# Optimization experiments

Hardware: AMD Instinct MI355X
Metric: run time of the kernel (lower is better)

Reference implementation:

```python
import jax, jax.numpy as jnp
import numpy as np

D = 1024
H = 16
FF = 4 * D


def layer_norm(x, g, b, eps=1e-5):
    mu = jnp.mean(x, axis=-1, keepdims=True)
    var = jnp.var(x, axis=-1, keepdims=True)
    return (x - mu) * jax.lax.rsqrt(var + eps) * g + b


def setup_inputs() -> dict:
    key = jax.random.key(0)
    ks = jax.random.split(key, 8)
    s = lambda fan_in: 1.0 / np.sqrt(fan_in)
    return {
        "x": jax.random.normal(ks[0], (2, 2048, D), dtype=jnp.float32),
        "ln1_g": jnp.ones((D,), jnp.float32),
        "ln1_b": jnp.zeros((D,), jnp.float32),
        "w_qkv": jax.random.uniform(ks[1], (D, 3 * D), jnp.float32, -s(D), s(D)),
        "b_qkv": jnp.zeros((3 * D,), jnp.float32),
        "w_out": jax.random.uniform(ks[2], (D, D), jnp.float32, -s(D), s(D)),
        "b_out": jnp.zeros((D,), jnp.float32),
        "ln2_g": jnp.ones((D,), jnp.float32),
        "ln2_b": jnp.zeros((D,), jnp.float32),
        "w_fc1": jax.random.uniform(ks[3], (D, FF), jnp.float32, -s(D), s(D)),
        "b_fc1": jnp.zeros((FF,), jnp.float32),
        "w_fc2": jax.random.uniform(ks[4], (FF, D), jnp.float32, -s(FF), s(FF)),
        "b_fc2": jnp.zeros((D,), jnp.float32),
    }


def reference(x, ln1_g, ln1_b, w_qkv, b_qkv, w_out, b_out,
              ln2_g, ln2_b, w_fc1, b_fc1, w_fc2, b_fc2):
    b, n, c = x.shape
    hd = c // H
    scale = hd ** -0.5

    # --- pre-norm MHA ---
    h = layer_norm(x, ln1_g, ln1_b)
    qkv = h @ w_qkv + b_qkv                      # [b,n,3c]
    qkv = qkv.reshape(b, n, 3, H, hd)
    q = jnp.transpose(qkv[:, :, 0], (0, 2, 1, 3))  # [b,H,n,hd]
    k = jnp.transpose(qkv[:, :, 1], (0, 2, 1, 3))
    v = jnp.transpose(qkv[:, :, 2], (0, 2, 1, 3))
    attn = jnp.einsum('bhqd,bhkd->bhqk', q, k) * scale
    attn = jax.nn.softmax(attn, axis=-1)
    o = jnp.einsum('bhqk,bhkd->bhqd', attn, v)   # [b,H,n,hd]
    o = jnp.transpose(o, (0, 2, 1, 3)).reshape(b, n, c)
    x = x + (o @ w_out + b_out)

    # --- pre-norm FFN ---
    h = layer_norm(x, ln2_g, ln2_b)
    h = jax.nn.gelu(h @ w_fc1 + b_fc1, approximate=False)
    x = x + (h @ w_fc2 + b_fc2)
    return x
```

## Files before the change

### kernel.cpp

```cpp
#include <hip/hip_runtime.h>
#include <stdint.h>
#include <math.h>

#define D_MODEL 1024
#define NHEAD   16
#define HDIM    64
#define FFDIM   4096
#define SEQ     2048
#define BATCH   2
#define NTOK    (BATCH*SEQ)
#define QKVN    (3*D_MODEL)

typedef __bf16 bf16;
typedef __attribute__((ext_vector_type(8))) __bf16 bf16x8;
typedef __attribute__((ext_vector_type(4))) __bf16 bf16x4;
typedef __attribute__((ext_vector_type(4))) float f32x4;

__device__ __forceinline__ void gld_lds16(const void* g, void* l) {
    __builtin_amdgcn_global_load_lds((__attribute__((address_space(1))) void*)g,
                                     (__attribute__((address_space(3))) void*)l,
                                     16, 0, 0);
}

__device__ __forceinline__ float fast_exp2(float x) {
#if __has_builtin(__builtin_amdgcn_exp2f)
    return __builtin_amdgcn_exp2f(x);
#else
    return __expf(x * 0.69314718056f);
#endif
}

__device__ __forceinline__ float fast_rcp(float x) {
#if __has_builtin(__builtin_amdgcn_rcpf)
    return __builtin_amdgcn_rcpf(x);
#else
    return 1.0f / x;
#endif
}

__device__ __forceinline__ float gelu_fast(float x) {
    float xx = x * x;
    float y  = x * fmaf(0.035677408137f, xx, 0.7978845608f);
    float z  = fminf(-2.8853900817779268f * y, 126.0f);
    float e  = fast_exp2(z);
    return x * fast_rcp(1.0f + e);
}

#define PHASE_BAR() do {                                       \
    asm volatile("s_waitcnt vmcnt(0)" ::: "memory");           \
    __builtin_amdgcn_s_barrier();                              \
    asm volatile("" ::: "memory");                             \
} while (0)

#define GEMM_BAR() do {                                        \
    asm volatile("s_waitcnt lgkmcnt(0)" ::: "memory");         \
    __builtin_amdgcn_s_barrier();                              \
    asm volatile("" ::: "memory");                             \
} while (0)

__global__ __launch_bounds__(256)
void k_transpose_all(const float* __restrict__ w_qkv, const float* __restrict__ w_out,
                     const float* __restrict__ w_fc1, const float* __restrict__ w_fc2,
                     bf16* __restrict__ t_qkv, bf16* __restrict__ t_out,
                     bf16* __restrict__ t_fc1, bf16* __restrict__ t_fc2) {
    __shared__ float tile[32][33];
    int bid = blockIdx.x;
    const float* W; bf16* Wt; int K, N, ti;
    if (bid < 3072)       { W = w_qkv; Wt = t_qkv; K = 1024; N = 3072; ti = bid; }
    else if (bid < 4096)  { W = w_out; Wt = t_out; K = 1024; N = 1024; ti = bid - 3072; }
    else if (bid < 8192)  { W = w_fc1; Wt = t_fc1; K = 1024; N = 4096; ti = bid - 4096; }
    else                  { W = w_fc2; Wt = t_fc2; K = 4096; N = 1024; ti = bid - 8192; }
    int tn = N >> 5;
    int n0 = (ti % tn) * 32, k0 = (ti / tn) * 32;
    int tx = threadIdx.x, ty = threadIdx.y;
#pragma unroll
    for (int i = 0; i < 4; i++)
        tile[ty + i * 8][tx] = W[(size_t)(k0 + ty + i * 8) * N + n0 + tx];
    __syncthreads();
#pragma unroll
    for (int i = 0; i < 4; i++)
        Wt[(size_t)(n0 + ty + i * 8) * K + k0 + tx] = (bf16)tile[tx][ty + i * 8];
}

__global__ __launch_bounds__(256)
void k_vtrans(const bf16* __restrict__ qkv, bf16* __restrict__ vT) {
    __shared__ bf16 t[32][33];
    int tok0 = blockIdx.x * 32, f0 = blockIdx.y * 32;
    int tx = threadIdx.x, ty = threadIdx.y;
#pragma unroll
    for (int i = 0; i < 4; i++)
        t[ty + i * 8][tx] = qkv[(size_t)(tok0 + ty + i * 8) * QKVN + 2 * D_MODEL + f0 + tx];
    __syncthreads();
    int s = tx;
    int pp = (s < 16) ? ((s >> 2) * 8 + (s & 3))
                      : (((s - 16) >> 2) * 8 + ((s - 16) & 3) + 4);
#pragma unroll
    for (int i = 0; i < 4; i++)
        vT[(size_t)(f0 + ty + i * 8) * NTOK + tok0 + pp] = t[tx][ty + i * 8];
}

__global__ __launch_bounds__(256)
void k_layernorm(const float* __restrict__ x, const float* __restrict__ g,
                 const float* __restrict__ b, bf16* __restrict__ out) {
    int row = blockIdx.x;
    int tid = threadIdx.x;
    float4 v = ((const float4*)(x + (size_t)row * D_MODEL))[tid];
    float s  = v.x + v.y + v.z + v.w;
    float ss = v.x * v.x + v.y * v.y + v.z * v.z + v.w * v.w;
#pragma unroll
    for (int off = 32; off > 0; off >>= 1) {
        s  += __shfl_down(s, off, 64);
        ss += __shfl_down(ss, off, 64);
    }
    __shared__ float red[2][4];
    __shared__ float mv[2];
    int wave = tid >> 6, lane = tid & 63;
    if (lane == 0) { red[0][wave] = s; red[1][wave] = ss; }
    __syncthreads();
    if (tid == 0) {
        float S  = red[0][0] + red[0][1] + red[0][2] + red[0][3];
        float SS = red[1][0] + red[1][1] + red[1][2] + red[1][3];
        float mu = S * (1.0f / D_MODEL);
        float var = SS * (1.0f / D_MODEL) - mu * mu;
        mv[0] = mu;
        mv[1] = rsqrtf(var + 1e-5f);
    }
    __syncthreads();
    float mu = mv[0], rs = mv[1];
    float4 gv = ((const float4*)g)[tid];
    float4 bv = ((const float4*)b)[tid];
    bf16x4 ov = { (bf16)((v.x - mu) * rs * gv.x + bv.x),
                  (bf16)((v.y - mu) * rs * gv.y + bv.y),
                  (bf16)((v.z - mu) * rs * gv.z + bv.z),
                  (bf16)((v.w - mu) * rs * gv.w + bv.w) };
    *(bf16x4*)(out + (size_t)row * D_MODEL + tid * 4) = ov;
}

template <int DO_GELU, int DO_RES, int OUT_BF16, int BN, int PIPE2, int SPLITK, int STAGE>
__global__ __launch_bounds__(256)
void k_gemm(const bf16* __restrict__ A, const bf16* __restrict__ Bt,
            const float* __restrict__ bias, const float* __restrict__ res,
            float* __restrict__ outf, bf16* __restrict__ outb,
            int M, int N, int K) {
    constexpr int WN = BN / 32;
    __shared__ bf16 As[2][128 * 32];
    __shared__ bf16 Bs[2][BN * 32];
    int tid  = threadIdx.x;
    int wave = tid >> 6, lane = tid & 63;
    int quad = lane >> 4, l16 = lane & 15;

    int nwg = gridDim.x * gridDim.y;
    int bid = blockIdx.y * gridDim.x + blockIdx.x;
    int sid = (bid & 7) * (nwg >> 3) + (bid >> 3);
    int bx = sid % gridDim.x, by = sid / gridDim.x;
    int m0 = by * 128, n0 = bx * BN;
    int wm = (wave >> 1) * 64, wn = (wave & 1) * (BN / 2);

    int Keff = (SPLITK == 2) ? (K >> 1) : K;
    int koff = (SPLITK == 2) ? blockIdx.z * Keff : 0;

    f32x4 acc[4][WN];
#pragma unroll
    for (int i = 0; i < 4; i++)
#pragma unroll
        for (int j = 0; j < WN; j++) acc[i][j] = (f32x4){0.f, 0.f, 0.f, 0.f};

    int lrow = lane >> 2;
    int lcol = (lane & 3) * 8;
    const bf16* gA0 = A + (size_t)(m0 + wave * 32 + lrow) * K + koff + lcol;
    const bf16* gA1 = gA0 + (size_t)16 * K;
    const bf16* gB0;
    const bf16* gB1 = nullptr;
    if constexpr (BN == 128) {
        gB0 = Bt + (size_t)(n0 + wave * 32 + lrow) * K + koff + lcol;
        gB1 = gB0 + (size_t)16 * K;
    } else {
        gB0 = Bt + (size_t)(n0 + wave * 16 + lrow) * K + koff + lcol;
    }

    int wA0 = wave * 1024 + lane * 8;
    int wA1 = wA0 + 512;
    int wB0 = (BN == 128) ? (wave * 1024 + lane * 8) : (wave * 512 + lane * 8);
    int wB1 = wB0 + 512;

    auto issue = [&](bf16x8* r, int k0) {
        r[0] = *(const bf16x8*)(gA0 + k0);
        r[1] = *(const bf16x8*)(gA1 + k0);
        r[2] = *(const bf16x8*)(gB0 + k0);
        if constexpr (BN == 128) r[3] = *(const bf16x8*)(gB1 + k0);
    };
    auto commit = [&](int buf, const bf16x8* r) {
        *(bf16x8*)(&As[buf][wA0]) = r[0];
        *(bf16x8*)(&As[buf][wA1]) = r[1];
        *(bf16x8*)(&Bs[buf][wB0]) = r[2];
        if constexpr (BN == 128) *(bf16x8*)(&Bs[buf][wB1]) = r[3];
    };
    auto compute = [&](const bf16* cA, const bf16* cB) {
        bf16x8 af[4], bfr[WN];
#pragma unroll
        for (int mi = 0; mi < 4; mi++)
            af[mi] = *(const bf16x8*)(cA + (wm + mi * 16 + l16) * 32 + quad * 8);
#pragma unroll
        for (int ni = 0; ni < WN; ni++)
            bfr[ni] = *(const bf16x8*)(cB + (wn + ni * 16 + l16) * 32 + quad * 8);
#pragma unroll
        for (int mi = 0; mi < 4; mi++)
#pragma unroll
            for (int ni = 0; ni < WN; ni++)
                acc[mi][ni] = __builtin_amdgcn_mfma_f32_16x16x32_bf16(af[mi], bfr[ni], acc[mi][ni], 0, 0, 0);
    };

    int niter = Keff / 32;

    if constexpr (STAGE == 1) {
        bf16* sA  = &As[0][wave * 1024];
        bf16* sB  = &Bs[0][(BN == 128) ? wave * 1024 : wave * 512];
        bf16* sA2 = &As[1][wave * 1024];
        bf16* sB2 = &Bs[1][(BN == 128) ? wave * 1024 : wave * 512];
        const bf16* rA  = &As[0][0]; const bf16* rB  = &Bs[0][0];
        const bf16* rA2 = &As[1][0]; const bf16* rB2 = &Bs[1][0];
        gld_lds16(gA0, sA);
        gld_lds16(gA1, sA + 512);
        gld_lds16(gB0, sB);
        if constexpr (BN == 128) gld_lds16(gB1, sB + 512);
        PHASE_BAR();
        for (int t = 1; t < niter; t++) {
            int k0 = t * 32;
            gld_lds16(gA0 + k0, sA2);
            gld_lds16(gA1 + k0, sA2 + 512);
            gld_lds16(gB0 + k0, sB2);
            if constexpr (BN == 128) gld_lds16(gB1 + k0, sB2 + 512);
            compute(rA, rB);
            PHASE_BAR();
            bf16* t0 = sA; sA = sA2; sA2 = t0;
            bf16* t1 = sB; sB = sB2; sB2 = t1;
            const bf16* t2 = rA; rA = rA2; rA2 = t2;
            const bf16* t3 = rB; rB = rB2; rB2 = t3;
        }
        compute(rA, rB);
    } else if constexpr (!PIPE2) {
        bf16x8 r0[4];
        issue(r0, 0);
        commit(0, r0);
        __syncthreads();
        for (int t = 1; t < niter; t++) {
            issue(r0, t * 32);
            compute(&As[(t - 1) & 1][0], &Bs[(t - 1) & 1][0]);
            commit(t & 1, r0);
            __syncthreads();
        }
        compute(&As[(niter - 1) & 1][0], &Bs[(niter - 1) & 1][0]);
    } else {
        bf16x8 r0[4], r1[4];
        issue(r0, 0);
        commit(0, r0);
        issue(r1, 32);
        GEMM_BAR();
        for (int t = 1; t + 2 < niter; t += 2) {
            issue(r0, (t + 1) * 32);
            compute(&As[0][0], &Bs[0][0]);
            commit(1, r1);
            GEMM_BAR();
            issue(r1, (t + 2) * 32);
            compute(&As[1][0], &Bs[1][0]);
            commit(0, r0);
            GEMM_BAR();
        }
        compute(&As[0][0], &Bs[0][0]);
        commit(1, r1);
        GEMM_BAR();
        compute(&As[1][0], &Bs[1][0]);
    }

#pragma unroll
    for (int mi = 0; mi < 4; mi++) {
        int row = m0 + wm + mi * 16 + quad * 4;
#pragma unroll
        for (int ni = 0; ni < WN; ni++) {
            int col = n0 + wn + ni * 16 + l16;
            if constexpr (SPLITK == 2) {
                float bb = (blockIdx.z == 0) ? bias[col] : 0.0f;
#pragma unroll
                for (int r = 0; r < 4; r++)
                    atomicAdd(&outf[(size_t)(row + r) * N + col], acc[mi][ni][r] + bb);
                continue;
            }
            float bb = bias[col];
#pragma unroll
            for (int r = 0; r < 4; r++) {
                float v = acc[mi][ni][r] + bb;
                if (DO_GELU) v = gelu_fast(v);
                size_t idx = (size_t)(row + r) * N + col;
                if (DO_RES) v += res[idx];
                if (OUT_BF16) outb[idx] = (bf16)v;
                else          outf[idx] = v;
            }
        }
    }
}

__global__ __launch_bounds__(256)
void k_attention2(const bf16* __restrict__ qkv, const bf16* __restrict__ vT,
                  bf16* __restrict__ o) {
    __shared__ bf16 Ks[2][2][64][32];
    __shared__ bf16 Vs[2][2][64][32];

    int tid = threadIdx.x, wave = tid >> 6, lane = tid & 63;
    int quad = lane >> 4, l16 = lane & 15;
    int bh = blockIdx.y;
    int b = bh >> 4, h = bh & 15;
    int q0 = blockIdx.x * 64 + wave * 16;

    const bf16* Qb  = qkv + (size_t)b * SEQ * QKVN + h * HDIM;
    const bf16* Kb  = Qb + D_MODEL;
    const bf16* vTb = vT + (size_t)h * HDIM * NTOK + b * SEQ;

    const float QSCALE = 0.125f * 1.44269504089f;
    bf16x8 qf[2];
#pragma unroll
    for (int c = 0; c < 2; c++) {
        bf16x8 qraw = *(const bf16x8*)(Qb + (size_t)(q0 + l16) * QKVN + c * 32 + quad * 8);
#pragma unroll
        for (int i = 0; i < 8; i++) qf[c][i] = (bf16)((float)qraw[i] * QSCALE);
    }

    const bf16* gK0 = Kb + (size_t)(wave * 16 + (lane >> 2)) * QKVN + (lane & 3) * 8;
    const bf16* gK1 = gK0 + 32;
    const bf16* gV0 = vTb + (size_t)(wave * 16 + (lane >> 2)) * NTOK + (lane & 3) * 8;
    const bf16* gV1 = gV0 + 32;

    f32x4 oacc[4];
#pragma unroll
    for (int i = 0; i < 4; i++) oacc[i] = (f32x4){0.f, 0.f, 0.f, 0.f};
    float lsum = 0.f;

    {
        gld_lds16(gK0, &Ks[0][0][wave * 16][0]);
        gld_lds16(gK1, &Ks[0][1][wave * 16][0]);
        gld_lds16(gV0, &Vs[0][0][wave * 16][0]);
        gld_lds16(gV1, &Vs[0][1][wave * 16][0]);
    }
    PHASE_BAR();

    int buf = 0;
    for (int kv0 = 0; kv0 < SEQ; kv0 += 64) {
        if (kv0 + 64 < SEQ) {
            size_t koff = (size_t)(kv0 + 64) * QKVN;
            gld_lds16(gK0 + koff, &Ks[buf ^ 1][0][wave * 16][0]);
            gld_lds16(gK1 + koff, &Ks[buf ^ 1][1][wave * 16][0]);
            gld_lds16(gV0 + kv0 + 64, &Vs[buf ^ 1][0][wave * 16][0]);
            gld_lds16(gV1 + kv0 + 64, &Vs[buf ^ 1][1][wave * 16][0]);
        }

        f32x4 s[4];
#pragma unroll
        for (int t = 0; t < 4; t++) {
            bf16x8 af0 = *(const bf16x8*)(&Ks[buf][0][t * 16 + l16][quad * 8]);
            bf16x8 af1 = *(const bf16x8*)(&Ks[buf][1][t * 16 + l16][quad * 8]);
            f32x4 z = (f32x4){0.f, 0.f, 0.f, 0.f};
            z = __builtin_amdgcn_mfma_f32_16x16x32_bf16(af0, qf[0], z, 0, 0, 0);
            z = __builtin_amdgcn_mfma_f32_16x16x32_bf16(af1, qf[1], z, 0, 0, 0);
            s[t] = z;
        }

        bf16x4 p[4];
#pragma unroll
        for (int t = 0; t < 4; t++)
#pragma unroll
            for (int r = 0; r < 4; r++) {
                float pf = fast_exp2(s[t][r]);
                lsum += pf;
                p[t][r] = (bf16)pf;
            }

#pragma unroll
        for (int tp = 0; tp < 2; tp++) {
            bf16x8 pa = __builtin_shufflevector(p[2 * tp], p[2 * tp + 1], 0, 1, 2, 3, 4, 5, 6, 7);
#pragma unroll
            for (int nt = 0; nt < 4; nt++) {
                bf16x8 vb = *(const bf16x8*)(&Vs[buf][tp][nt * 16 + l16][quad * 8]);
                oacc[nt] = __builtin_amdgcn_mfma_f32_16x16x32_bf16(pa, vb, oacc[nt], 0, 0, 0);
            }
        }

        PHASE_BAR();
        buf ^= 1;
    }

    lsum += __shfl_xor(lsum, 16, 64);
    lsum += __shfl_xor(lsum, 32, 64);
    float invl[4];
#pragma unroll
    for (int r = 0; r < 4; r++)
        invl[r] = 1.0f / __shfl(lsum, quad * 4 + r, 16);

#pragma unroll
    for (int nt = 0; nt < 4; nt++)
#pragma unroll
        for (int r = 0; r < 4; r++)
            o[(size_t)(b * SEQ + q0 + quad * 4 + r) * D_MODEL + h * HDIM + nt * 16 + l16] =
                (bf16)(oacc[nt][r] * invl[r]);
}

extern "C" void kernel_launch(void* const* d_in, const int* in_sizes, int n_in,
                              void* d_out, int out_size, void* d_ws, size_t ws_size,
                              hipStream_t stream) {
    const float* x     = (const float*)d_in[0];
    const float* ln1_g = (const float*)d_in[1];
    const float* ln1_b = (const float*)d_in[2];
    const float* w_qkv = (const float*)d_in[3];
    const float* b_qkv = (const float*)d_in[4];
    const float* w_out = (const float*)d_in[5];
    const float* b_out = (const float*)d_in[6];
    const float* ln2_g = (const float*)d_in[7];
    const float* ln2_b = (const float*)d_in[8];
    const float* w_fc1 = (const float*)d_in[9];
    const float* b_fc1 = (const float*)d_in[10];
    const float* w_fc2 = (const float*)d_in[11];
    const float* b_fc2 = (const float*)d_in[12];
    float* out = (float*)d_out;

    uintptr_t ws = (uintptr_t)d_ws;
    bf16* wt_qkv = (bf16*)(ws + 0);
    bf16* wt_out = (bf16*)(ws + 6291456);
    bf16* wt_fc1 = (bf16*)(ws + 8388608);
    bf16* wt_fc2 = (bf16*)(ws + 16777216);
    bf16* hbuf   = (bf16*)(ws + 25165824);
    bf16* vT     = hbuf;
    bf16* qkv    = (bf16*)(ws + 33554432);
    bf16* attn_o = (bf16*)(ws + 58720256);
    bf16* hgelu  = (bf16*)(ws + 33554432);

    k_transpose_all<<<12288, dim3(32, 8), 0, stream>>>(w_qkv, w_out, w_fc1, w_fc2,
                                                       wt_qkv, wt_out, wt_fc1, wt_fc2);

    k_layernorm<<<NTOK, 256, 0, stream>>>(x, ln1_g, ln1_b, hbuf);

    k_gemm<0, 0, 1, 128, 0, 1, 1><<<dim3(QKVN / 128, NTOK / 128), 256, 0, stream>>>(
        hbuf, wt_qkv, b_qkv, nullptr, nullptr, qkv, NTOK, QKVN, D_MODEL);

    k_vtrans<<<dim3(NTOK / 32, D_MODEL / 32), dim3(32, 8), 0, stream>>>(qkv, vT);

    k_attention2<<<dim3(SEQ / 64, BATCH * NHEAD), 256, 0, stream>>>(qkv, vT, attn_o);

    k_gemm<0, 1, 0, 64, 1, 1, 0><<<dim3(D_MODEL / 64, NTOK / 128), 256, 0, stream>>>(
        attn_o, wt_out, b_out, x, out, nullptr, NTOK, D_MODEL, D_MODEL);

    k_layernorm<<<NTOK, 256, 0, stream>>>(out, ln2_g, ln2_b, hbuf);

    k_gemm<1, 0, 1, 128, 0, 1, 1><<<dim3(FFDIM / 128, NTOK / 128), 256, 0, stream>>>(
        hbuf, wt_fc1, b_fc1, nullptr, nullptr, hgelu, NTOK, FFDIM, D_MODEL);

    k_gemm<0, 0, 0, 128, 1, 2, 0><<<dim3(D_MODEL / 128, NTOK / 128, 2), 256, 0, stream>>>(
        hgelu, wt_fc2, b_fc2, nullptr, out, nullptr, NTOK, D_MODEL, FFDIM);
}
```

Baseline: 358.8 us.

## Add 256x256-tile 512-thread GEMM with swizzled LDS for QKV and FC1

Introduces a new GEMM kernel using 256x256 output tiles across 8 waves, with XOR-swizzled LDS layout, double-buffered direct global-to-LDS loads split into K halves, partial vmcnt waits, and MFMA priority boosting. It replaces the 128x128 GEMM for the QKV projection and the FC1+GELU projection to raise data reuse per tile and cut LDS bank conflicts. Larger tiles reduce the number of workgroups (e.g. 192 for QKV), which may underfill the 256 CUs, and increase register pressure. The epilogue writes scalar bf16 stores.

```diff
diff --git a/kernel.cpp b/kernel.cpp
--- a/kernel.cpp
+++ b/kernel.cpp
@@ -45,6 +45,12 @@
     float e  = fast_exp2(z);
     return x * fast_rcp(1.0f + e);
 }
+
+#define SYNC_VM(N) do {                                        \
+    asm volatile("s_waitcnt vmcnt(" #N ")" ::: "memory");      \
+    __builtin_amdgcn_s_barrier();                              \
+    asm volatile("" ::: "memory");                             \
+} while (0)
 
 #define PHASE_BAR() do {                                       \
     asm volatile("s_waitcnt vmcnt(0)" ::: "memory");           \
@@ -136,6 +142,128 @@
     *(bf16x4*)(out + (size_t)row * D_MODEL + tid * 4) = ov;
 }
 
+template <int DO_GELU>
+__global__ __launch_bounds__(512, 2)
+void k_gemm256(const bf16* __restrict__ A, const bf16* __restrict__ Bt,
+               const float* __restrict__ bias, bf16* __restrict__ outb,
+               int M, int N, int K) {
+    __shared__ bf16 LA[2][2][8192];
+    __shared__ bf16 LB[2][2][8192];
+
+    int tid = threadIdx.x;
+    int wid = tid >> 6, lane = tid & 63;
+    int quad = lane >> 4, l16 = lane & 15;
+    int wm = (wid >> 2) * 128;
+    int wn = (wid & 3) * 64;
+
+    int nwg = gridDim.x * gridDim.y;
+    int bid = blockIdx.y * gridDim.x + blockIdx.x;
+    int sid = (bid & 7) * (nwg >> 3) + (bid >> 3);
+    int bx = sid % gridDim.x, by = sid / gridDim.x;
+    int m0 = by * 256, n0 = bx * 256;
+
+    int l = lane;
+    int rsw = l >> 2;
+    int csw = 8 * ((l & 3) ^ ((l >> 3) & 3));
+    const bf16* pA = A  + (size_t)(m0 + 32 * wid + rsw) * K + csw;
+    const bf16* pB = Bt + (size_t)(n0 + 32 * wid + rsw) * K + csw;
+    int sbase = wid * 1024;
+
+    int xq = 8 * (quad ^ ((l16 >> 1) & 3));
+
+    f32x4 acc[8][4];
+#pragma unroll
+    for (int i = 0; i < 8; i++)
+#pragma unroll
+        for (int j = 0; j < 4; j++) acc[i][j] = (f32x4){0.f, 0.f, 0.f, 0.f};
+
+#define STAGE_A(buf, kh, t) do {                                               \
+    gld_lds16(pA + (size_t)(t) * 64 + (kh) * 32,              &LA[buf][kh][sbase]);       \
+    gld_lds16(pA + (size_t)16 * K + (size_t)(t) * 64 + (kh) * 32, &LA[buf][kh][sbase + 512]); \
+} while (0)
+#define STAGE_B(buf, kh, t) do {                                               \
+    gld_lds16(pB + (size_t)(t) * 64 + (kh) * 32,              &LB[buf][kh][sbase]);       \
+    gld_lds16(pB + (size_t)16 * K + (size_t)(t) * 64 + (kh) * 32, &LB[buf][kh][sbase + 512]); \
+} while (0)
+
+    bf16x8 af[4], bfr[4];
+#define RD_B(buf, kh)  do {                                                    \
+    _Pragma("unroll")                                                          \
+    for (int fc = 0; fc < 4; fc++)                                             \
+        bfr[fc] = *(const bf16x8*)&LB[buf][kh][(wn + fc * 16 + l16) * 32 + xq];\
+} while (0)
+#define RD_A(buf, kh, rh) do {                                                 \
+    _Pragma("unroll")                                                          \
+    for (int fr = 0; fr < 4; fr++)                                             \
+        af[fr] = *(const bf16x8*)&LA[buf][kh][(wm + (rh) * 64 + fr * 16 + l16) * 32 + xq]; \
+} while (0)
+#define MFMA16(rh) do {                                                        \
+    __builtin_amdgcn_s_setprio(1);                                             \
+    _Pragma("unroll")                                                          \
+    for (int fr = 0; fr < 4; fr++)                                             \
+        _Pragma("unroll")                                                      \
+        for (int fc = 0; fc < 4; fc++)                                         \
+            acc[(rh) * 4 + fr][fc] =                                           \
+                __builtin_amdgcn_mfma_f32_16x16x32_bf16(af[fr], bfr[fc],       \
+                                                        acc[(rh) * 4 + fr][fc], 0, 0, 0); \
+    __builtin_amdgcn_s_setprio(0);                                             \
+} while (0)
+
+    int nt = K / 64;
+    int buf = 0;
+    STAGE_A(0, 0, 0); STAGE_B(0, 0, 0); STAGE_A(0, 1, 0); STAGE_B(0, 1, 0);
+
+    for (int t = 0; t < nt - 1; t++) {
+        SYNC_VM(4);
+        STAGE_A(buf ^ 1, 0, t + 1);
+        RD_B(buf, 0); RD_A(buf, 0, 0);
+        STAGE_B(buf ^ 1, 0, t + 1);
+        MFMA16(0);
+        RD_A(buf, 0, 1);
+        MFMA16(1);
+        SYNC_VM(4);
+        STAGE_A(buf ^ 1, 1, t + 1);
+        RD_B(buf, 1); RD_A(buf, 1, 0);
+        STAGE_B(buf ^ 1, 1, t + 1);
+        MFMA16(0);
+        RD_A(buf, 1, 1);
+        MFMA16(1);
+        buf ^= 1;
+    }
+    SYNC_VM(4);
+    RD_B(buf, 0); RD_A(buf, 0, 0);
+    MFMA16(0);
+    RD_A(buf, 0, 1);
+    MFMA16(1);
+    SYNC_VM(0);
+    RD_B(buf, 1); RD_A(buf, 1, 0);
+    MFMA16(0);
+    RD_A(buf, 1, 1);
+    MFMA16(1);
+
+#undef STAGE_A
+#undef STAGE_B
+#undef RD_A
+#undef RD_B
+#undef MFMA16
+
+#pragma unroll
+    for (int fi = 0; fi < 8; fi++) {
+        int row = m0 + wm + fi * 16 + quad * 4;
+#pragma unroll
+        for (int fc = 0; fc < 4; fc++) {
+            int col = n0 + wn + fc * 16 + l16;
+            float bb = bias[col];
+#pragma unroll
+            for (int r = 0; r < 4; r++) {
+                float v = acc[fi][fc][r] + bb;
+                if (DO_GELU) v = gelu_fast(v);
+                outb[(size_t)(row + r) * N + col] = (bf16)v;
+            }
+        }
+    }
+}
+
 template <int DO_GELU, int DO_RES, int OUT_BF16, int BN, int PIPE2, int SPLITK, int STAGE>
 __global__ __launch_bounds__(256)
 void k_gemm(const bf16* __restrict__ A, const bf16* __restrict__ Bt,
@@ -211,7 +339,6 @@
     };
 
     int niter = Keff / 32;
-
     if constexpr (STAGE == 1) {
         bf16* sA  = &As[0][wave * 1024];
         bf16* sB  = &Bs[0][(BN == 128) ? wave * 1024 : wave * 512];
@@ -334,12 +461,10 @@
     for (int i = 0; i < 4; i++) oacc[i] = (f32x4){0.f, 0.f, 0.f, 0.f};
     float lsum = 0.f;
 
-    {
-        gld_lds16(gK0, &Ks[0][0][wave * 16][0]);
-        gld_lds16(gK1, &Ks[0][1][wave * 16][0]);
-        gld_lds16(gV0, &Vs[0][0][wave * 16][0]);
-        gld_lds16(gV1, &Vs[0][1][wave * 16][0]);
-    }
+    gld_lds16(gK0, &Ks[0][0][wave * 16][0]);
+    gld_lds16(gK1, &Ks[0][1][wave * 16][0]);
+    gld_lds16(gV0, &Vs[0][0][wave * 16][0]);
+    gld_lds16(gV1, &Vs[0][1][wave * 16][0]);
     PHASE_BAR();
 
     int buf = 0;
@@ -436,8 +561,8 @@
 
     k_layernorm<<<NTOK, 256, 0, stream>>>(x, ln1_g, ln1_b, hbuf);
 
-    k_gemm<0, 0, 1, 128, 0, 1, 1><<<dim3(QKVN / 128, NTOK / 128), 256, 0, stream>>>(
-        hbuf, wt_qkv, b_qkv, nullptr, nullptr, qkv, NTOK, QKVN, D_MODEL);
+    k_gemm256<0><<<dim3(QKVN / 256, NTOK / 256), 512, 0, stream>>>(
+        hbuf, wt_qkv, b_qkv, qkv, NTOK, QKVN, D_MODEL);
 
     k_vtrans<<<dim3(NTOK / 32, D_MODEL / 32), dim3(32, 8), 0, stream>>>(qkv, vT);
 
@@ -448,8 +573,8 @@
 
     k_layernorm<<<NTOK, 256, 0, stream>>>(out, ln2_g, ln2_b, hbuf);
 
-    k_gemm<1, 0, 1, 128, 0, 1, 1><<<dim3(FFDIM / 128, NTOK / 128), 256, 0, stream>>>(
-        hbuf, wt_fc1, b_fc1, nullptr, nullptr, hgelu, NTOK, FFDIM, D_MODEL);
+    k_gemm256<1><<<dim3(FFDIM / 256, NTOK / 256), 512, 0, stream>>>(
+        hbuf, wt_fc1, b_fc1, hgelu, NTOK, FFDIM, D_MODEL);
 
     k_gemm<0, 0, 0, 128, 1, 2, 0><<<dim3(D_MODEL / 128, NTOK / 128, 2), 256, 0, stream>>>(
         hgelu, wt_fc2, b_fc2, nullptr, out, nullptr, NTOK, D_MODEL, FFDIM);
```

Result: no change. 353.3 us (-1.5%).
